# Kernel optimization log

Hardware: AMD Instinct MI355X
Metric: run time of the kernel (lower is better)

The kernel has to match this reference:

```python
import jax, jax.numpy as jnp
import numpy as np

ALPHA = 0.2  # leaky relu slope
NEG = -1e9


def setup_inputs() -> dict:
    key = jax.random.key(0)
    ks = jax.random.split(key, 8)
    B, N, F_IN, H, HID, OUT = 2, 4096, 512, 4, 128, 64
    x = jax.random.normal(ks[0], (B, N, F_IN), dtype=jnp.float32)
    adj = jax.random.randint(ks[1], (B, N, N), 0, 2, dtype=jnp.int32)
    s_in = float(np.sqrt(2.0 / (F_IN + HID)))
    W_heads = jax.random.normal(ks[2], (H, HID, F_IN), dtype=jnp.float32) * s_in
    a1_heads = jax.random.normal(ks[3], (H, HID), dtype=jnp.float32) * 0.1
    a2_heads = jax.random.normal(ks[4], (H, HID), dtype=jnp.float32) * 0.1
    s_out = float(np.sqrt(2.0 / (H * HID + OUT)))
    W_out = jax.random.normal(ks[5], (OUT, H * HID), dtype=jnp.float32) * s_out
    a1_out = jax.random.normal(ks[6], (OUT,), dtype=jnp.float32) * 0.1
    a2_out = jax.random.normal(ks[7], (OUT,), dtype=jnp.float32) * 0.1
    return {"x": x, "adj": adj, "W_heads": W_heads, "a1_heads": a1_heads,
            "a2_heads": a2_heads, "W_out": W_out, "a1_out": a1_out, "a2_out": a2_out}


def _gat_layer(x, adj, W, a1, a2, concat):
    # x: [B,N,F], W: [O,F], a1/a2: [O]
    h = jnp.einsum('bnf,of->bno', x, W)            # [B,N,O]
    f1 = jnp.einsum('bno,o->bn', h, a1)            # [B,N]
    f2 = jnp.einsum('bno,o->bn', h, a2)            # [B,N]
    e = f1[:, :, None] + f2[:, None, :]            # [B,N,N] additive scores
    e = jnp.where(e > 0, e, ALPHA * e)             # leaky relu
    e = jnp.where(adj == 0, NEG, e)                # adjacency mask
    att = jax.nn.softmax(e, axis=2)
    h_prime = jnp.einsum('bnm,bmo->bno', att, h)
    return jax.nn.elu(h_prime) if concat else h_prime


def reference(x, adj, W_heads, a1_heads, a2_heads, W_out, a1_out, a2_out):
    H = W_heads.shape[0]
    heads = [_gat_layer(x, adj, W_heads[i], a1_heads[i], a2_heads[i], True)
             for i in range(H)]
    x_cat = jnp.concatenate(heads, axis=2)         # [B,N,H*HID]
    return _gat_layer(x_cat, adj, W_out, a1_out, a2_out, False)
```

## Files before the change

kernel.cpp:

```cpp
#include <hip/hip_runtime.h>

#define TB 2
#define TN 4096
#define TH 4
#define THID 128
#define TOUT 64
#define NW 128

using f4    = __attribute__((ext_vector_type(4))) float;
using s16x8 = __attribute__((ext_vector_type(8))) short;
using s16x4 = __attribute__((ext_vector_type(4))) short;
using u32x4 = __attribute__((ext_vector_type(4))) unsigned;

static __device__ __forceinline__ short f2bf(float f){
  unsigned u = __float_as_uint(f);
  unsigned r = u + 0x7FFFu + ((u >> 16) & 1u);
  return (short)(r >> 16);
}
static __device__ __forceinline__ float bf2f(short s){
  return __uint_as_float(((unsigned)(unsigned short)s) << 16);
}
static __device__ __forceinline__ unsigned encf(float f){
  unsigned u = __float_as_uint(f);
  return (u & 0x80000000u) ? ~u : (u | 0x80000000u);
}
static __device__ __forceinline__ float decf(unsigned u){
  unsigned v = (u & 0x80000000u) ? (u & 0x7FFFFFFFu) : ~u;
  return __uint_as_float(v);
}
static __device__ __forceinline__ void gll16(const void* g, void* l){
  __builtin_amdgcn_global_load_lds((const __attribute__((address_space(1))) unsigned int*)g,
                                   (__attribute__((address_space(3))) unsigned int*)l, 16, 0, 0);
}
static __device__ __forceinline__ f4 mfma_bf16(s16x8 a, s16x8 b, f4 c){
  return __builtin_amdgcn_mfma_f32_16x16x32_bf16(a, b, c, 0, 0, 0);
}

__global__ void k_pack(const int* __restrict__ adj, unsigned* __restrict__ adjT,
                       unsigned* __restrict__ mx){
  if (blockIdx.x == 0 && threadIdx.x < 16) mx[threadIdx.x] = 0;
  int t = blockIdx.x * 256 + threadIdx.x;
  int n = t & 4095, w = (t >> 12) & 127, b = t >> 19;
  const int4* p = (const int4*)(adj + ((size_t)(b*TN + n))*TN + w*32);
  unsigned m = 0;
#pragma unroll
  for (int i = 0; i < 8; ++i){
    int4 v = p[i];
    m |= (v.x != 0 ? 1u : 0u) << (i*4+0);
    m |= (v.y != 0 ? 1u : 0u) << (i*4+1);
    m |= (v.z != 0 ? 1u : 0u) << (i*4+2);
    m |= (v.w != 0 ? 1u : 0u) << (i*4+3);
  }
  adjT[((size_t)(b*NW + w))*TN + n] = m;
}

__global__ void k_split(const float* __restrict__ x, short* __restrict__ hi, short* __restrict__ lo){
  int t = blockIdx.x * 256 + threadIdx.x;
  f4 v = ((const f4*)x)[t];
  s16x4 h, l;
#pragma unroll
  for (int e = 0; e < 4; ++e){
    short hb = f2bf(v[e]);
    h[e] = hb;
    l[e] = f2bf(v[e] - bf2f(hb));
  }
  ((s16x4*)hi)[t] = h;
  ((s16x4*)lo)[t] = l;
}
__global__ void k_cvt(const float* __restrict__ x, short* __restrict__ o){
  int t = blockIdx.x * 256 + threadIdx.x;
  f4 v = ((const f4*)x)[t];
  s16x4 h;
#pragma unroll
  for (int e = 0; e < 4; ++e) h[e] = f2bf(v[e]);
  ((s16x4*)o)[t] = h;
}

__global__ __launch_bounds__(512, 2) void k_gemm1(
    const short* __restrict__ xh, const short* __restrict__ xl,
    const short* __restrict__ wh, const short* __restrict__ wl,
    const float* __restrict__ a1h, const float* __restrict__ a2h,
    short* __restrict__ hTb, float* __restrict__ f1g,
    float* __restrict__ Qa, float* __restrict__ Sa, unsigned* __restrict__ mx){
  __shared__ short tiles[2][4][8192];
  __shared__ float red[2][128][2];
  __shared__ float bmx[2];
  int tid = threadIdx.x, lane = tid & 63, w = tid >> 6;
  int kgrp = lane >> 4, li = lane & 15;
  int nblk = blockIdx.x >> 6, mblk = blockIdx.x & 63;
  int n0 = nblk * 128, m0 = mblk * 128;
  int wn = w >> 2, wm = w & 3;
  const f4 fz = {0.f, 0.f, 0.f, 0.f};
  f4 acc[4][2];
#pragma unroll
  for (int i = 0; i < 4; ++i)
#pragma unroll
    for (int j = 0; j < 2; ++j) acc[i][j] = fz;

#pragma unroll
  for (int tno = 0; tno < 4; ++tno){
    const short* gb = (tno==0 ? wh : tno==1 ? wl : tno==2 ? xh : xl);
    int r0 = (tno < 2) ? n0 : m0;
#pragma unroll
    for (int i = 0; i < 2; ++i){
      int s = (i*8 + w)*64 + lane;
      int row = s >> 3, c = s & 7, cs = c ^ (row & 7);
      gll16(gb + (size_t)(r0 + row)*512 + cs*8, (char*)tiles[0][tno] + (i*8+w)*1024);
    }
  }
  asm volatile("s_waitcnt vmcnt(0)" ::: "memory");
  __syncthreads();

  for (int kt = 0; kt < 8; ++kt){
    int cur = kt & 1;
    if (kt < 7){
      int k0 = (kt+1) * 64;
#pragma unroll
      for (int tno = 0; tno < 4; ++tno){
        const short* gb = (tno==0 ? wh : tno==1 ? wl : tno==2 ? xh : xl);
        int r0 = (tno < 2) ? n0 : m0;
#pragma unroll
        for (int i = 0; i < 2; ++i){
          int s = (i*8 + w)*64 + lane;
          int row = s >> 3, c = s & 7, cs = c ^ (row & 7);
          gll16(gb + (size_t)(r0 + row)*512 + k0 + cs*8, (char*)tiles[cur^1][tno] + (i*8+w)*1024);
        }
      }
    }
    const char* t0 = (const char*)tiles[cur][0];
    const char* t1 = (const char*)tiles[cur][1];
    const char* t2 = (const char*)tiles[cur][2];
    const char* t3 = (const char*)tiles[cur][3];
#pragma unroll
    for (int ks = 0; ks < 2; ++ks){
      int ck = ks*4 + kgrp;
      s16x8 ah[4], al[4], bh[2], bl[2];
#pragma unroll
      for (int fn = 0; fn < 4; ++fn){
        int row = wn*64 + fn*16 + li;
        int off = row*128 + ((ck ^ (row & 7)) << 4);
        ah[fn] = *(const s16x8*)(t0 + off);
        al[fn] = *(const s16x8*)(t1 + off);
      }
#pragma unroll
      for (int fm = 0; fm < 2; ++fm){
        int row = wm*32 + fm*16 + li;
        int off = row*128 + ((ck ^ (row & 7)) << 4);
        bh[fm] = *(const s16x8*)(t2 + off);
        bl[fm] = *(const s16x8*)(t3 + off);
      }
#pragma unroll
      for (int fn = 0; fn < 4; ++fn)
#pragma unroll
        for (int fm = 0; fm < 2; ++fm)
          acc[fn][fm] = mfma_bf16(ah[fn], bh[fm], acc[fn][fm]);
#pragma unroll
      for (int fn = 0; fn < 4; ++fn)
#pragma unroll
        for (int fm = 0; fm < 2; ++fm)
          acc[fn][fm] = mfma_bf16(ah[fn], bl[fm], acc[fn][fm]);
#pragma unroll
      for (int fn = 0; fn < 4; ++fn)
#pragma unroll
        for (int fm = 0; fm < 2; ++fm)
          acc[fn][fm] = mfma_bf16(al[fn], bh[fm], acc[fn][fm]);
    }
    asm volatile("s_waitcnt vmcnt(0)" ::: "memory");
    __syncthreads();
  }
  int head = nblk;
#pragma unroll
  for (int fn = 0; fn < 4; ++fn){
#pragma unroll
    for (int fm = 0; fm < 2; ++fm){
#pragma unroll
      for (int r = 0; r < 4; ++r){
        int nout = n0 + wn*64 + fn*16 + kgrp*4 + r;
        int m = m0 + wm*32 + fm*16 + li;
        int b = m >> 12, n = m & 4095;
        int hid = nout & 127;
        size_t idx = ((size_t)((b*TH + head)*THID + hid))*TN + n;
        hTb[idx] = f2bf(acc[fn][fm][r]);
      }
    }
  }
  const float* a1p = a1h + head*THID;
  const float* a2p = a2h + head*THID;
  float s1[2] = {0.f, 0.f}, s2[2] = {0.f, 0.f};
#pragma unroll
  for (int fn = 0; fn < 4; ++fn)
#pragma unroll
    for (int r = 0; r < 4; ++r){
      int row = wn*64 + fn*16 + kgrp*4 + r;
      float w1 = a1p[row], w2 = a2p[row];
#pragma unroll
      for (int fm = 0; fm < 2; ++fm){
        s1[fm] = fmaf(acc[fn][fm][r], w1, s1[fm]);
        s2[fm] = fmaf(acc[fn][fm][r], w2, s2[fm]);
      }
    }
#pragma unroll
  for (int fm = 0; fm < 2; ++fm){
    s1[fm] += __shfl_xor(s1[fm], 16); s1[fm] += __shfl_xor(s1[fm], 32);
    s2[fm] += __shfl_xor(s2[fm], 16); s2[fm] += __shfl_xor(s2[fm], 32);
  }
  if (kgrp == 0){
#pragma unroll
    for (int fm = 0; fm < 2; ++fm){
      int col = wm*32 + fm*16 + li;
      red[wn][col][0] = s1[fm];
      red[wn][col][1] = s2[fm];
    }
  }
  __syncthreads();
  if (tid < 128){
    float f1v = red[0][tid][0] + red[1][tid][0];
    float f2v = red[0][tid][1] + red[1][tid][1];
    int m = m0 + tid, b = m >> 12, n = m & 4095;
    int idx = (b*TH + head)*TN + n;
    f1g[idx] = f1v;
    Qa[idx] = expf(f2v);
    Sa[idx] = expf(0.2f*f2v);
    float wmx = f2v;
#pragma unroll
    for (int d = 1; d < 64; d <<= 1) wmx = fmaxf(wmx, __shfl_xor(wmx, d));
    if ((tid & 63) == 0) bmx[tid >> 6] = wmx;
  }
  __syncthreads();
  if (tid == 0){
    int b = m0 >> 12;
    atomicMax(&mx[b*TH + head], encf(fmaxf(bmx[0], bmx[1])));
  }
}

__global__ __launch_bounds__(256, 2) void k_attn1(
    const short* __restrict__ hTb, const float* __restrict__ f1,
    const float* __restrict__ Qa, const float* __restrict__ Sa,
    const unsigned* __restrict__ adjT, const unsigned* __restrict__ mx,
    short* __restrict__ part, float* __restrict__ sums){
  __shared__ short tile[3][8192];
  __shared__ float Qs[1024], Ss[1024];
  __shared__ unsigned abuf[3][512];
  int tid = threadIdx.x, lane = tid & 63, w = tid >> 6;
  int kgrp = lane >> 4, li = lane & 15;
  int bid = blockIdx.x;
  int js = bid >> 7, b = (bid >> 6) & 1, h = (bid >> 4) & 3, rblk = bid & 15;
  int bh = b*TH + h;
  int jbase = js * 1024;
  int r0b = rblk * 256;
  const short* hbase = hTb + ((size_t)bh*THID)*TN;
  const float* Qrow = Qa + (size_t)bh*TN + jbase;
  const float* Srow = Sa + (size_t)bh*TN + jbase;

  auto STAGE = [&](int t){
    int jg = jbase + t*64;
    int bi = t % 3;
    char* dst = (char*)tile[bi];
#pragma unroll
    for (int i = 0; i < 4; ++i){
      int s = (i*4 + w)*64 + lane;
      int row = s >> 3, c = s & 7, cs = c ^ (row & 7);
      gll16(hbase + (size_t)row*TN + jg + cs*8, dst + (i*4+w)*1024);
    }
    int w0 = jg >> 5;
#pragma unroll
    for (int k = 0; k < 2; ++k)
      gll16(adjT + (size_t)(b*NW + w0 + k)*TN + r0b + lane*4, (char*)abuf[bi] + k*1024);
  };

  gll16(Qrow + w*256 + lane*4, (char*)Qs + w*1024);
  gll16(Srow + w*256 + lane*4, (char*)Ss + w*1024);
  STAGE(0); STAGE(1);

  int r0 = r0b + w*64;
  float Pv[4], Rv[4];
  int lrow[4];
  float mf = decf(mx[bh]);
#pragma unroll
  for (int rf = 0; rf < 4; ++rf){
    int row = r0 + rf*16 + li;
    lrow[rf] = w*64 + rf*16 + li;
    float f1v = f1[bh*TN + row];
    float e = f1v + mf;
    float m = e > 0.f ? e : 0.2f*e;
    Pv[rf] = expf(f1v - m);
    Rv[rf] = expf(0.2f*f1v - m);
  }
  const f4 fz = {0.f,0.f,0.f,0.f};
  f4 acc[4][8];
#pragma unroll
  for (int i = 0; i < 4; ++i)
#pragma unroll
    for (int j = 0; j < 8; ++j) acc[i][j] = fz;
  f4 accs[4] = {fz, fz, fz, fz};
  s16x8 ones;
#pragma unroll
  for (int e = 0; e < 8; ++e) ones[e] = (short)0x3F80;

  for (int jt = 0; jt < 16; ++jt){
    if (jt < 15) asm volatile("s_waitcnt vmcnt(6)" ::: "memory");
    else         asm volatile("s_waitcnt vmcnt(0)" ::: "memory");
    __builtin_amdgcn_s_barrier();
    __builtin_amdgcn_sched_barrier(0);
    if (jt < 14) STAGE(jt + 2);

    int j0 = jt*64;
    int bi = jt % 3;
    const char* tp = (const char*)tile[bi];
    const unsigned* ab = abuf[bi];
    unsigned aw0[4], aw1[4];
#pragma unroll
    for (int rf = 0; rf < 4; ++rf){
      aw0[rf] = ab[lrow[rf]];
      aw1[rf] = ab[256 + lrow[rf]];
    }
#pragma unroll
    for (int ks = 0; ks < 2; ++ks){
      int jloc = j0 + ks*32 + kgrp*8;
      float qv[8], sv[8];
      *(f4*)&qv[0] = *(const f4*)&Qs[jloc];
      *(f4*)&qv[4] = *(const f4*)&Qs[jloc+4];
      *(f4*)&sv[0] = *(const f4*)&Ss[jloc];
      *(f4*)&sv[4] = *(const f4*)&Ss[jloc+4];
      s16x8 af[4];
#pragma unroll
      for (int rf = 0; rf < 4; ++rf){
        unsigned word = ks ? aw1[rf] : aw0[rf];
        unsigned byt = (word >> (kgrp*8)) & 0xFFu;
        float P = Pv[rf], R = Rv[rf];
        u32x4 pw;
#pragma unroll
        for (int pe = 0; pe < 4; ++pe){
          float va = fmaxf(P*qv[2*pe],   R*sv[2*pe]);
          float vb = fmaxf(P*qv[2*pe+1], R*sv[2*pe+1]);
          va = (byt & (1u << (2*pe)))   ? va : 0.f;
          vb = (byt & (1u << (2*pe+1))) ? vb : 0.f;
          unsigned ua = __float_as_uint(va) + 0x8000u;
          unsigned ub = __float_as_uint(vb) + 0x8000u;
          pw[pe] = __builtin_amdgcn_perm(ub, ua, 0x07060302);
        }
        af[rf] = __builtin_bit_cast(s16x8, pw);
      }
#pragma unroll
      for (int rf = 0; rf < 4; ++rf)
        accs[rf] = mfma_bf16(af[rf], ones, accs[rf]);
#pragma unroll
      for (int cf = 0; cf < 8; ++cf){
        int col = cf*16 + li;
        int off = col*128 + (((ks*4 + kgrp) ^ (col & 7)) << 4);
        s16x8 bfr = *(const s16x8*)(tp + off);
#pragma unroll
        for (int rf = 0; rf < 4; ++rf)
          acc[rf][cf] = mfma_bf16(af[rf], bfr, acc[rf][cf]);
      }
    }
  }
  int sl = js*8 + bh;
  if (li == 0){
#pragma unroll
    for (int rf = 0; rf < 4; ++rf)
#pragma unroll
      for (int r = 0; r < 4; ++r)
        sums[(size_t)sl*TN + r0 + rf*16 + kgrp*4 + r] = accs[rf][r];
  }
#pragma unroll
  for (int rf = 0; rf < 4; ++rf)
#pragma unroll
    for (int cf = 0; cf < 8; ++cf)
#pragma unroll
      for (int r = 0; r < 4; ++r){
        int row = r0 + rf*16 + kgrp*4 + r;
        int hid = cf*16 + li;
        part[((size_t)sl*TN + row)*THID + hid] = f2bf(acc[rf][cf][r]);
      }
}

__global__ void k_comb1(const short* __restrict__ part, const float* __restrict__ sums,
                        short* __restrict__ xcat){
  int t = blockIdx.x*256 + threadIdx.x;
  int hid8 = t & 15, n = (t >> 4) & 4095, h = (t >> 16) & 3, b = t >> 18;
  int bh = b*TH + h;
  float a[8] = {0,0,0,0,0,0,0,0};
  float s = 0.f;
#pragma unroll
  for (int js = 0; js < 4; ++js){
    size_t rowoff = (size_t)(js*8 + bh)*TN + n;
    s16x8 pv = *(const s16x8*)(part + rowoff*THID + hid8*8);
#pragma unroll
    for (int e = 0; e < 8; ++e) a[e] += bf2f(pv[e]);
    s += sums[rowoff];
  }
  float inv = 1.f / s;
  s16x8 o;
#pragma unroll
  for (int e = 0; e < 8; ++e){
    float x = a[e] * inv;
    o[e] = f2bf(x > 0.f ? x : expm1f(x));
  }
  *(s16x8*)(xcat + ((size_t)(b*TN + n))*512 + h*128 + hid8*8) = o;
}

__global__ __launch_bounds__(128) void k_gemm2(
    const short* __restrict__ xcat, const short* __restrict__ wo,
    const float* __restrict__ a1o, const float* __restrict__ a2o,
    short* __restrict__ h2T, float* __restrict__ f1o,
    float* __restrict__ Q2, float* __restrict__ S2, unsigned* __restrict__ mx2){
  int tid = threadIdx.x, lane = tid & 63, w = tid >> 6;
  int kgrp = lane >> 4, li = lane & 15;
  int m0 = blockIdx.x * 32;
  const f4 fz = {0.f,0.f,0.f,0.f};
  f4 acc[4] = {fz, fz, fz, fz};
  int rowA = m0 + w*16 + li;
  for (int kt = 0; kt < 16; ++kt){
    int k = kt*32 + kgrp*8;
    s16x8 a = *(const s16x8*)(xcat + (size_t)rowA*512 + k);
#pragma unroll
    for (int cf = 0; cf < 4; ++cf){
      int col = cf*16 + li;
      s16x8 bfr = *(const s16x8*)(wo + (size_t)col*512 + k);
      acc[cf] = mfma_bf16(a, bfr, acc[cf]);
    }
  }
  float p1[4] = {0,0,0,0}, p2[4] = {0,0,0,0};
#pragma unroll
  for (int cf = 0; cf < 4; ++cf){
    int o = cf*16 + li;
    float w1 = a1o[o], w2 = a2o[o];
#pragma unroll
    for (int r = 0; r < 4; ++r){
      p1[r] = fmaf(acc[cf][r], w1, p1[r]);
      p2[r] = fmaf(acc[cf][r], w2, p2[r]);
    }
  }
#pragma unroll
  for (int r = 0; r < 4; ++r){
#pragma unroll
    for (int d = 1; d < 16; d <<= 1){
      p1[r] += __shfl_xor(p1[r], d);
      p2[r] += __shfl_xor(p2[r], d);
    }
  }
#pragma unroll
  for (int cf = 0; cf < 4; ++cf)
#pragma unroll
    for (int r = 0; r < 4; ++r){
      int row = m0 + w*16 + kgrp*4 + r;
      int o = cf*16 + li;
      int b = row >> 12, n = row & 4095;
      h2T[((size_t)(b*TOUT + o))*TN + n] = f2bf(acc[cf][r]);
    }
  if (li == 0){
#pragma unroll
    for (int r = 0; r < 4; ++r){
      int row = m0 + w*16 + kgrp*4 + r;
      f1o[row] = p1[r];
      Q2[row] = expf(p2[r]);
      S2[row] = expf(0.2f*p2[r]);
    }
  }
  float m2 = fmaxf(fmaxf(p2[0], p2[1]), fmaxf(p2[2], p2[3]));
  m2 = fmaxf(m2, __shfl_xor(m2, 16));
  m2 = fmaxf(m2, __shfl_xor(m2, 32));
  __shared__ float bm[2];
  if (lane == 0) bm[w] = m2;
  __syncthreads();
  if (tid == 0) atomicMax(&mx2[m0 >> 12], encf(fmaxf(bm[0], bm[1])));
}

__global__ __launch_bounds__(256, 2) void k_attn2(
    const short* __restrict__ h2T, const float* __restrict__ f1o,
    const float* __restrict__ Q2, const float* __restrict__ S2,
    const unsigned* __restrict__ adjT, const unsigned* __restrict__ mx2,
    float* __restrict__ part, float* __restrict__ sums){
  __shared__ short tile[3][4096];
  __shared__ float Qs[512], Ss[512];
  __shared__ unsigned abuf[3][256];
  int tid = threadIdx.x, lane = tid & 63, w = tid >> 6;
  int kgrp = lane >> 4, li = lane & 15;
  int bid = blockIdx.x;
  int js = bid >> 6, b = (bid >> 5) & 1, rblk = bid & 31;
  int jbase = js * 512;
  int r0b = rblk * 128;
  const short* hbase = h2T + (size_t)b*TOUT*TN;
  const float* Qrow = Q2 + (size_t)b*TN + jbase;
  const float* Srow = S2 + (size_t)b*TN + jbase;

  auto STAGE = [&](int t){
    int jg = jbase + t*64;
    int bi = t % 3;
    char* dst = (char*)tile[bi];
#pragma unroll
    for (int i = 0; i < 2; ++i){
      int s = (i*4 + w)*64 + lane;
      int row = s >> 3, c = s & 7, cs = c ^ (row & 7);
      gll16(hbase + (size_t)row*TN + jg + cs*8, dst + (i*4+w)*1024);
    }
    int w0 = jg >> 5;
    gll16(adjT + (size_t)(b*NW + w0 + (lane>>5))*TN + r0b + (lane&31)*4, (char*)abuf[bi]);
  };

  if (w < 2) gll16(Qrow + w*256 + lane*4, (char*)Qs + w*1024);
  else       gll16(Srow + (w-2)*256 + lane*4, (char*)Ss + (w-2)*1024);
  STAGE(0); STAGE(1);

  int r0 = r0b + w*32;
  float Pv[2], Rv[2];
  int lrow[2];
  float mf = decf(mx2[b]);
#pragma unroll
  for (int rf = 0; rf < 2; ++rf){
    int row = r0 + rf*16 + li;
    lrow[rf] = w*32 + rf*16 + li;
    float f1v = f1o[b*TN + row];
    float e = f1v + mf;
    float m = e > 0.f ? e : 0.2f*e;
    Pv[rf] = expf(f1v - m);
    Rv[rf] = expf(0.2f*f1v - m);
  }
  const f4 fz = {0.f,0.f,0.f,0.f};
  f4 acc[2][4];
#pragma unroll
  for (int i = 0; i < 2; ++i)
#pragma unroll
    for (int j = 0; j < 4; ++j) acc[i][j] = fz;
  f4 accs[2] = {fz, fz};
  s16x8 ones;
#pragma unroll
  for (int e = 0; e < 8; ++e) ones[e] = (short)0x3F80;

  for (int jt = 0; jt < 8; ++jt){
    if (jt < 7) asm volatile("s_waitcnt vmcnt(3)" ::: "memory");
    else        asm volatile("s_waitcnt vmcnt(0)" ::: "memory");
    __builtin_amdgcn_s_barrier();
    __builtin_amdgcn_sched_barrier(0);
    if (jt < 6) STAGE(jt + 2);

    int j0 = jt*64;
    int bi = jt % 3;
    const char* tp = (const char*)tile[bi];
    const unsigned* ab = abuf[bi];
    unsigned aw0[2], aw1[2];
#pragma unroll
    for (int rf = 0; rf < 2; ++rf){
      aw0[rf] = ab[lrow[rf]];
      aw1[rf] = ab[128 + lrow[rf]];
    }
#pragma unroll
    for (int ks = 0; ks < 2; ++ks){
      int jloc = j0 + ks*32 + kgrp*8;
      float qv[8], sv[8];
      *(f4*)&qv[0] = *(const f4*)&Qs[jloc];
      *(f4*)&qv[4] = *(const f4*)&Qs[jloc+4];
      *(f4*)&sv[0] = *(const f4*)&Ss[jloc];
      *(f4*)&sv[4] = *(const f4*)&Ss[jloc+4];
      s16x8 af[2];
#pragma unroll
      for (int rf = 0; rf < 2; ++rf){
        unsigned word = ks ? aw1[rf] : aw0[rf];
        unsigned byt = (word >> (kgrp*8)) & 0xFFu;
        float P = Pv[rf], R = Rv[rf];
        u32x4 pw;
#pragma unroll
        for (int pe = 0; pe < 4; ++pe){
          float va = fmaxf(P*qv[2*pe],   R*sv[2*pe]);
          float vb = fmaxf(P*qv[2*pe+1], R*sv[2*pe+1]);
          va = (byt & (1u << (2*pe)))   ? va : 0.f;
          vb = (byt & (1u << (2*pe+1))) ? vb : 0.f;
          unsigned ua = __float_as_uint(va) + 0x8000u;
          unsigned ub = __float_as_uint(vb) + 0x8000u;
          pw[pe] = __builtin_amdgcn_perm(ub, ua, 0x07060302);
        }
        af[rf] = __builtin_bit_cast(s16x8, pw);
      }
      accs[0] = mfma_bf16(af[0], ones, accs[0]);
      accs[1] = mfma_bf16(af[1], ones, accs[1]);
#pragma unroll
      for (int cf = 0; cf < 4; ++cf){
        int col = cf*16 + li;
        int off = col*128 + (((ks*4 + kgrp) ^ (col & 7)) << 4);
        s16x8 bfr = *(const s16x8*)(tp + off);
        acc[0][cf] = mfma_bf16(af[0], bfr, acc[0][cf]);
        acc[1][cf] = mfma_bf16(af[1], bfr, acc[1][cf]);
      }
    }
  }
  int sl = js*2 + b;
  if (li == 0){
#pragma unroll
    for (int rf = 0; rf < 2; ++rf)
#pragma unroll
      for (int r = 0; r < 4; ++r)
        sums[(size_t)sl*TN + r0 + rf*16 + kgrp*4 + r] = accs[rf][r];
  }
#pragma unroll
  for (int rf = 0; rf < 2; ++rf)
#pragma unroll
    for (int cf = 0; cf < 4; ++cf)
#pragma unroll
      for (int r = 0; r < 4; ++r){
        int row = r0 + rf*16 + kgrp*4 + r;
        int o = cf*16 + li;
        part[((size_t)sl*TN + row)*TOUT + o] = acc[rf][cf][r];
      }
}

__global__ void k_comb2(const float* __restrict__ part, const float* __restrict__ sums,
                        float* __restrict__ out){
  int t = blockIdx.x*256 + threadIdx.x;
  int o4 = t & 15, n = (t >> 4) & 4095, b = t >> 16;
  f4 a = {0.f,0.f,0.f,0.f};
  float s = 0.f;
#pragma unroll
  for (int js = 0; js < 8; ++js){
    int sl = js*2 + b;
    a += ((const f4*)part)[((size_t)sl*TN + n)*16 + o4];
    s += sums[(size_t)sl*TN + n];
  }
  f4 r = a / s;
  ((f4*)out)[((size_t)(b*TN + n))*16 + o4] = r;
}

extern "C" void kernel_launch(void* const* d_in, const int* in_sizes, int n_in,
                              void* d_out, int out_size, void* d_ws, size_t ws_size,
                              hipStream_t stream) {
  (void)in_sizes; (void)n_in; (void)out_size; (void)ws_size;
  const float* x       = (const float*)d_in[0];
  const int*   adj     = (const int*)d_in[1];
  const float* W_heads = (const float*)d_in[2];
  const float* a1h     = (const float*)d_in[3];
  const float* a2h     = (const float*)d_in[4];
  const float* W_out   = (const float*)d_in[5];
  const float* a1o     = (const float*)d_in[6];
  const float* a2o     = (const float*)d_in[7];

  char* p = (char*)d_ws;
  auto alloc = [&](size_t sz){ char* r = p; p += (sz + 255) & ~(size_t)255; return r; };
  unsigned* adjT  = (unsigned*) alloc(4ull*1048576);
  short*    wo    = (short*)    alloc(2ull*32768);
  short*    hTb   = (short*)    alloc(2ull*4194304);
  float*    f1    = (float*)    alloc(4ull*32768);
  float*    Qa    = (float*)    alloc(4ull*32768);
  float*    Sa    = (float*)    alloc(4ull*32768);
  unsigned* mx    = (unsigned*) alloc(4ull*16);
  short*    xcat  = (short*)    alloc(2ull*4194304);
  float*    f1o   = (float*)    alloc(4ull*8192);
  float*    Q2    = (float*)    alloc(4ull*8192);
  float*    S2    = (float*)    alloc(4ull*8192);
  short*    h2T   = (short*)    alloc(2ull*524288);
  float*    sums1 = (float*)    alloc(4ull*131072);
  float*    sums2 = (float*)    alloc(4ull*65536);
  char* A = alloc(33554432ull);
  short* xh   = (short*)A;
  short* xl   = (short*)(A + 8388608);
  short* part1 = (short*)A;
  char* Bu = alloc(16777216ull);
  short* wh = (short*)Bu;
  short* wl = (short*)(Bu + 524288);
  float* part2 = (float*)Bu;

  k_pack <<<4096, 256, 0, stream>>>(adj, adjT, mx);
  k_split<<<4096, 256, 0, stream>>>(x, xh, xl);
  k_split<<<256, 256, 0, stream>>>(W_heads, wh, wl);
  k_cvt  <<<32, 256, 0, stream>>>(W_out, wo);
  k_gemm1<<<256, 512, 0, stream>>>(xh, xl, wh, wl, a1h, a2h, hTb, f1, Qa, Sa, mx);
  k_attn1<<<512, 256, 0, stream>>>(hTb, f1, Qa, Sa, adjT, mx, part1, sums1);
  k_comb1<<<2048, 256, 0, stream>>>(part1, sums1, xcat);
  k_gemm2<<<256, 128, 0, stream>>>(xcat, wo, a1o, a2o, h2T, f1o, Q2, S2, mx + 8);
  k_attn2<<<512, 256, 0, stream>>>(h2T, f1o, Q2, S2, adjT, mx + 8, part2, sums2);
  k_comb2<<<512, 256, 0, stream>>>(part2, sums2, (float*)d_out);
}
```

Before: 148.0 us.

## Fuse prep kernels into one launch and merge combine-1 into gemm2 via LDS

Merges the four preprocessing kernels (adjacency pack, x split, W_heads split, W_out convert) into one launch that dispatches on block index. It also folds the head-combine step (partial sum reduction, normalisation, ELU) into the second GEMM: each block builds its 32x512 bf16 activation tile in swizzled shared memory instead of reading a global xcat buffer. This removes several launches and the xcat write/read round trip. The cost is that combine work now runs on only 256 small blocks of 128 threads, which lowers parallelism for that phase, and a leftover dummy sums1 read loop adds a little overhead.

After: 150.4 us. Within noise of the previous version (+1.6%).

```diff
diff --git a/kernel.cpp b/kernel.cpp
--- a/kernel.cpp
+++ b/kernel.cpp
@@ -36,44 +36,59 @@
   return __builtin_amdgcn_mfma_f32_16x16x32_bf16(a, b, c, 0, 0, 0);
 }
 
-__global__ void k_pack(const int* __restrict__ adj, unsigned* __restrict__ adjT,
-                       unsigned* __restrict__ mx){
-  if (blockIdx.x == 0 && threadIdx.x < 16) mx[threadIdx.x] = 0;
-  int t = blockIdx.x * 256 + threadIdx.x;
-  int n = t & 4095, w = (t >> 12) & 127, b = t >> 19;
-  const int4* p = (const int4*)(adj + ((size_t)(b*TN + n))*TN + w*32);
-  unsigned m = 0;
-#pragma unroll
-  for (int i = 0; i < 8; ++i){
-    int4 v = p[i];
-    m |= (v.x != 0 ? 1u : 0u) << (i*4+0);
-    m |= (v.y != 0 ? 1u : 0u) << (i*4+1);
-    m |= (v.z != 0 ? 1u : 0u) << (i*4+2);
-    m |= (v.w != 0 ? 1u : 0u) << (i*4+3);
-  }
-  adjT[((size_t)(b*NW + w))*TN + n] = m;
-}
-
-__global__ void k_split(const float* __restrict__ x, short* __restrict__ hi, short* __restrict__ lo){
-  int t = blockIdx.x * 256 + threadIdx.x;
-  f4 v = ((const f4*)x)[t];
-  s16x4 h, l;
-#pragma unroll
-  for (int e = 0; e < 4; ++e){
-    short hb = f2bf(v[e]);
-    h[e] = hb;
-    l[e] = f2bf(v[e] - bf2f(hb));
-  }
-  ((s16x4*)hi)[t] = h;
-  ((s16x4*)lo)[t] = l;
-}
-__global__ void k_cvt(const float* __restrict__ x, short* __restrict__ o){
-  int t = blockIdx.x * 256 + threadIdx.x;
-  f4 v = ((const f4*)x)[t];
-  s16x4 h;
-#pragma unroll
-  for (int e = 0; e < 4; ++e) h[e] = f2bf(v[e]);
-  ((s16x4*)o)[t] = h;
+__global__ void k_prep(const int* __restrict__ adj, unsigned* __restrict__ adjT,
+                       unsigned* __restrict__ mx,
+                       const float* __restrict__ x, short* __restrict__ xh, short* __restrict__ xl,
+                       const float* __restrict__ Wh, short* __restrict__ wh, short* __restrict__ wl,
+                       const float* __restrict__ Wo, short* __restrict__ wo){
+  int bid = blockIdx.x;
+  if (bid == 0 && threadIdx.x < 16) mx[threadIdx.x] = 0;
+  if (bid < 4096){
+    int t = bid * 256 + threadIdx.x;
+    int n = t & 4095, w = (t >> 12) & 127, b = t >> 19;
+    const int4* p = (const int4*)(adj + ((size_t)(b*TN + n))*TN + w*32);
+    unsigned m = 0;
+#pragma unroll
+    for (int i = 0; i < 8; ++i){
+      int4 v = p[i];
+      m |= (v.x != 0 ? 1u : 0u) << (i*4+0);
+      m |= (v.y != 0 ? 1u : 0u) << (i*4+1);
+      m |= (v.z != 0 ? 1u : 0u) << (i*4+2);
+      m |= (v.w != 0 ? 1u : 0u) << (i*4+3);
+    }
+    adjT[((size_t)(b*NW + w))*TN + n] = m;
+  } else if (bid < 8192){
+    int t = (bid - 4096) * 256 + threadIdx.x;
+    f4 v = ((const f4*)x)[t];
+    s16x4 h, l;
+#pragma unroll
+    for (int e = 0; e < 4; ++e){
+      short hb = f2bf(v[e]);
+      h[e] = hb;
+      l[e] = f2bf(v[e] - bf2f(hb));
+    }
+    ((s16x4*)xh)[t] = h;
+    ((s16x4*)xl)[t] = l;
+  } else if (bid < 8448){
+    int t = (bid - 8192) * 256 + threadIdx.x;
+    f4 v = ((const f4*)Wh)[t];
+    s16x4 h, l;
+#pragma unroll
+    for (int e = 0; e < 4; ++e){
+      short hb = f2bf(v[e]);
+      h[e] = hb;
+      l[e] = f2bf(v[e] - bf2f(hb));
+    }
+    ((s16x4*)wh)[t] = h;
+    ((s16x4*)wl)[t] = l;
+  } else {
+    int t = (bid - 8448) * 256 + threadIdx.x;
+    f4 v = ((const f4*)Wo)[t];
+    s16x4 h;
+#pragma unroll
+    for (int e = 0; e < 4; ++e) h[e] = f2bf(v[e]);
+    ((s16x4*)wo)[t] = h;
+  }
 }
 
 __global__ __launch_bounds__(512, 2) void k_gemm1(
@@ -375,45 +390,57 @@
       }
 }
 
-__global__ void k_comb1(const short* __restrict__ part, const float* __restrict__ sums,
-                        short* __restrict__ xcat){
-  int t = blockIdx.x*256 + threadIdx.x;
-  int hid8 = t & 15, n = (t >> 4) & 4095, h = (t >> 16) & 3, b = t >> 18;
-  int bh = b*TH + h;
-  float a[8] = {0,0,0,0,0,0,0,0};
-  float s = 0.f;
-#pragma unroll
-  for (int js = 0; js < 4; ++js){
-    size_t rowoff = (size_t)(js*8 + bh)*TN + n;
-    s16x8 pv = *(const s16x8*)(part + rowoff*THID + hid8*8);
-#pragma unroll
-    for (int e = 0; e < 8; ++e) a[e] += bf2f(pv[e]);
-    s += sums[rowoff];
-  }
-  float inv = 1.f / s;
-  s16x8 o;
-#pragma unroll
-  for (int e = 0; e < 8; ++e){
-    float x = a[e] * inv;
-    o[e] = f2bf(x > 0.f ? x : expm1f(x));
-  }
-  *(s16x8*)(xcat + ((size_t)(b*TN + n))*512 + h*128 + hid8*8) = o;
-}
-
-__global__ __launch_bounds__(128) void k_gemm2(
-    const short* __restrict__ xcat, const short* __restrict__ wo,
+__global__ __launch_bounds__(128) void k_cg2(
+    const short* __restrict__ part1, const float* __restrict__ sums1,
+    const short* __restrict__ wo,
     const float* __restrict__ a1o, const float* __restrict__ a2o,
     short* __restrict__ h2T, float* __restrict__ f1o,
     float* __restrict__ Q2, float* __restrict__ S2, unsigned* __restrict__ mx2){
+  __shared__ short xs[32*512];
+  __shared__ float invs[32];
   int tid = threadIdx.x, lane = tid & 63, w = tid >> 6;
   int kgrp = lane >> 4, li = lane & 15;
   int m0 = blockIdx.x * 32;
+  if (tid < 32){
+    int row = m0 + tid, b = row >> 12, n = row & 4095;
+    float s = 0.f;
+#pragma unroll
+    for (int js = 0; js < 4; ++js)
+      s += sums1[(size_t)(js*8 + b*TH)*TN + 0];
+    (void)s; (void)n;
+  }
+  __syncthreads();
+  for (int it = 0; it < 16; ++it){
+    int idx = it*128 + tid;
+    int r = idx >> 6, c8 = idx & 63;
+    int row = m0 + r, b = row >> 12, n = row & 4095;
+    int h = c8 >> 4, hid8 = c8 & 15;
+    float a[8] = {0,0,0,0,0,0,0,0};
+    float s = 0.f;
+#pragma unroll
+    for (int js = 0; js < 4; ++js){
+      size_t rowoff = (size_t)(js*8 + b*TH + h)*TN + n;
+      s16x8 pv = *(const s16x8*)(part1 + rowoff*THID + hid8*8);
+#pragma unroll
+      for (int e = 0; e < 8; ++e) a[e] += bf2f(pv[e]);
+      s += sums1[rowoff];
+    }
+    float inv = 1.f / s;
+    s16x8 o;
+#pragma unroll
+    for (int e = 0; e < 8; ++e){
+      float xv = a[e] * inv;
+      o[e] = f2bf(xv > 0.f ? xv : expm1f(xv));
+    }
+    *(s16x8*)((char*)xs + r*1024 + ((c8*16) ^ ((r & 7) << 4))) = o;
+  }
+  __syncthreads();
   const f4 fz = {0.f,0.f,0.f,0.f};
   f4 acc[4] = {fz, fz, fz, fz};
-  int rowA = m0 + w*16 + li;
+  int rowL = w*16 + li;
   for (int kt = 0; kt < 16; ++kt){
     int k = kt*32 + kgrp*8;
-    s16x8 a = *(const s16x8*)(xcat + (size_t)rowA*512 + k);
+    s16x8 a = *(const s16x8*)((const char*)xs + rowL*1024 + ((k*2) ^ ((rowL & 7) << 4)));
 #pragma unroll
     for (int cf = 0; cf < 4; ++cf){
       int col = cf*16 + li;
@@ -465,6 +492,7 @@
   if (lane == 0) bm[w] = m2;
   __syncthreads();
   if (tid == 0) atomicMax(&mx2[m0 >> 12], encf(fmaxf(bm[0], bm[1])));
+  (void)invs;
 }
 
 __global__ __launch_bounds__(256, 2) void k_attn2(
@@ -642,7 +670,6 @@
   float*    Qa    = (float*)    alloc(4ull*32768);
   float*    Sa    = (float*)    alloc(4ull*32768);
   unsigned* mx    = (unsigned*) alloc(4ull*16);
-  short*    xcat  = (short*)    alloc(2ull*4194304);
   float*    f1o   = (float*)    alloc(4ull*8192);
   float*    Q2    = (float*)    alloc(4ull*8192);
   float*    S2    = (float*)    alloc(4ull*8192);
@@ -658,14 +685,10 @@
   short* wl = (short*)(Bu + 524288);
   float* part2 = (float*)Bu;
 
-  k_pack <<<4096, 256, 0, stream>>>(adj, adjT, mx);
-  k_split<<<4096, 256, 0, stream>>>(x, xh, xl);
-  k_split<<<256, 256, 0, stream>>>(W_heads, wh, wl);
-  k_cvt  <<<32, 256, 0, stream>>>(W_out, wo);
+  k_prep <<<8480, 256, 0, stream>>>(adj, adjT, mx, x, xh, xl, W_heads, wh, wl, W_out, wo);
   k_gemm1<<<256, 512, 0, stream>>>(xh, xl, wh, wl, a1h, a2h, hTb, f1, Qa, Sa, mx);
   k_attn1<<<512, 256, 0, stream>>>(hTb, f1, Qa, Sa, adjT, mx, part1, sums1);
-  k_comb1<<<2048, 256, 0, stream>>>(part1, sums1, xcat);
-  k_gemm2<<<256, 128, 0, stream>>>(xcat, wo, a1o, a2o, h2T, f1o, Q2, S2, mx + 8);
+  k_cg2  <<<256, 128, 0, stream>>>(part1, sums1, wo, a1o, a2o, h2T, f1o, Q2, S2, mx + 8);
   k_attn2<<<512, 256, 0, stream>>>(h2T, f1o, Q2, S2, adjT, mx + 8, part2, sums2);
   k_comb2<<<512, 256, 0, stream>>>(part2, sums2, (float*)d_out);
 }
```
